# Performance work log

Hardware: AMD Instinct MI355X
Metric: run time of the kernel (lower is better)

The kernel has to match this reference:

```python
import jax, jax.numpy as jnp
import numpy as np

N = 50000          # nodes
E = 800000         # edges
D_IN, D_HID, D_OUT = 256, 128, 64
NUM_GRAPHS = 16
BN_EPS = 1e-5


def gcn_conv(x, src, dst, W, b, n_nodes):
    """PyG GCNConv: add self-loops, sym-normalized aggregation, then bias."""
    loop = jnp.arange(n_nodes, dtype=src.dtype)
    s = jnp.concatenate([src, loop])
    d = jnp.concatenate([dst, loop])
    deg = jax.ops.segment_sum(jnp.ones_like(s, dtype=x.dtype), d, num_segments=n_nodes)
    dinv = jax.lax.rsqrt(jnp.maximum(deg, 1.0))  # deg >= 1 due to self-loops
    norm = dinv[s] * dinv[d]                      # [E+N]
    h = x @ W                                     # [N, out]
    msg = h[s] * norm[:, None]                    # gather + scale
    out = jax.ops.segment_sum(msg, d, num_segments=n_nodes)
    return out + b


def batch_norm(x, gamma, beta):
    mu = jnp.mean(x, axis=0)
    var = jnp.mean(jnp.square(x - mu), axis=0)
    return (x - mu) * jax.lax.rsqrt(var + BN_EPS) * gamma + beta


def setup_inputs() -> dict:
    key = jax.random.key(0)
    ks = jax.random.split(key, 10)
    x = jax.random.normal(ks[0], (N, D_IN), dtype=jnp.float32)
    edge_index = jax.random.randint(ks[1], (2, E), 0, N, dtype=jnp.int64)
    batch = jnp.sort(jax.random.randint(ks[2], (N,), 0, NUM_GRAPHS, dtype=jnp.int64))
    def glorot(k, fan_in, fan_out):
        lim = np.sqrt(6.0 / (fan_in + fan_out))
        return jax.random.uniform(k, (fan_in, fan_out), jnp.float32, -lim, lim)
    return {
        "x": x, "edge_index": edge_index, "batch": batch,
        "W1": glorot(ks[3], D_IN, D_HID),  "b1": jnp.zeros((D_HID,), jnp.float32),
        "W2": glorot(ks[4], D_HID, D_HID), "b2": jnp.zeros((D_HID,), jnp.float32),
        "W3": glorot(ks[5], D_HID, D_OUT), "b3": jnp.zeros((D_OUT,), jnp.float32),
        "g1": jnp.ones((D_HID,), jnp.float32), "be1": jnp.zeros((D_HID,), jnp.float32),
        "g2": jnp.ones((D_HID,), jnp.float32), "be2": jnp.zeros((D_HID,), jnp.float32),
    }


def reference(x, edge_index, batch, W1, b1, W2, b2, W3, b3, g1, be1, g2, be2):
    src, dst = edge_index[0], edge_index[1]
    n = x.shape[0]
    h = gcn_conv(x, src, dst, W1, b1, n)
    h = jax.nn.relu(batch_norm(h, g1, be1))
    h = gcn_conv(h, src, dst, W2, b2, n)
    h = jax.nn.relu(batch_norm(h, g2, be2))
    h = gcn_conv(h, src, dst, W3, b3, n)          # [N, D_OUT]
    # global mean pool over graph ids
    sums = jax.ops.segment_sum(h, batch, num_segments=NUM_GRAPHS)
    cnts = jax.ops.segment_sum(jnp.ones((n,), h.dtype), batch, num_segments=NUM_GRAPHS)
    return sums / jnp.maximum(cnts, 1.0)[:, None]  # [NUM_GRAPHS, D_OUT]
```

## Files before the change

kernel.cpp:

```cpp
#include <hip/hip_runtime.h>
#include <hip/hip_bf16.h>

#define D_IN   256
#define D_HID  128
#define D_OUT_ 64
#define NGRAPH 16
#define BN_EPS 1e-5f

#define SCAN_TPB 256
#define SCAN_VPT 4

typedef __attribute__((ext_vector_type(8))) short short8;
typedef __attribute__((ext_vector_type(4))) float floatx4;

__device__ __forceinline__ unsigned short f2bf(float x) {
    unsigned u = __float_as_uint(x);
    return (unsigned short)((u + 0x7fffu + ((u >> 16) & 1u)) >> 16);
}
__device__ __forceinline__ unsigned pack2bf(float lo, float hi) {
    return (unsigned)f2bf(lo) | ((unsigned)f2bf(hi) << 16);
}
__device__ __forceinline__ void bf2_decode(unsigned u, float& lo, float& hi) {
    lo = __uint_as_float(u << 16);
    hi = __uint_as_float(u & 0xffff0000u);
}
__device__ __forceinline__ void add8(float* acc, uint4 qv) {
    float f0,f1,f2,f3,f4,f5,f6,f7;
    bf2_decode(qv.x, f0, f1); bf2_decode(qv.y, f2, f3);
    bf2_decode(qv.z, f4, f5); bf2_decode(qv.w, f6, f7);
    acc[0]+=f0; acc[1]+=f1; acc[2]+=f2; acc[3]+=f3;
    acc[4]+=f4; acc[5]+=f5; acc[6]+=f6; acc[7]+=f7;
}

__global__ void prep_count_kernel(const float* __restrict__ W1, const float* __restrict__ W2,
                                  const float* __restrict__ W3,
                                  unsigned short* __restrict__ Wt1,
                                  unsigned short* __restrict__ Wt2,
                                  unsigned short* __restrict__ Wt3, int WB,
                                  const int* __restrict__ dst, int E,
                                  int* __restrict__ deg, int* __restrict__ rank) {
    if ((int)blockIdx.x < WB) {
        int idx = blockIdx.x * 256 + threadIdx.x;
        const int S1 = D_IN * D_HID;
        const int S2 = D_HID * D_HID;
        const int S3 = D_HID * D_OUT_;
        if (idx < S1) {
            int k = idx / D_HID, n = idx - k * D_HID;
            Wt1[(size_t)n * D_IN + k] = f2bf(W1[idx]);
        } else if (idx < S1 + S2) {
            int i = idx - S1;
            int k = i / D_HID, n = i - k * D_HID;
            Wt2[(size_t)n * D_HID + k] = f2bf(W2[i]);
        } else if (idx < S1 + S2 + S3) {
            int i = idx - S1 - S2;
            int k = i / D_OUT_, n = i - k * D_OUT_;
            Wt3[(size_t)n * D_HID + k] = f2bf(W3[i]);
        }
    } else {
        int e0 = ((int)blockIdx.x - WB) * (256 * 4) + threadIdx.x;
        int d[4];
        #pragma unroll
        for (int i = 0; i < 4; ++i) {
            int e = e0 + i * 256;
            if (e < E) d[i] = dst[e];
        }
        #pragma unroll
        for (int i = 0; i < 4; ++i) {
            int e = e0 + i * 256;
            if (e < E) rank[e] = atomicAdd(&deg[d[i]], 1);
        }
    }
}

__global__ void dinv_bsum_kernel(const int* __restrict__ deg, int N,
                                 float* __restrict__ dinv, int* __restrict__ bsum) {
    __shared__ int red[SCAN_TPB];
    int t = threadIdx.x;
    int base = blockIdx.x * (SCAN_TPB * SCAN_VPT) + t;
    int s = 0;
    #pragma unroll
    for (int i = 0; i < SCAN_VPT; ++i) {
        int idx = base + i * SCAN_TPB;
        if (idx < N) {
            int d = deg[idx];
            dinv[idx] = rsqrtf((float)(d + 1));
            s += d;
        }
    }
    red[t] = s;
    __syncthreads();
    for (int off = SCAN_TPB / 2; off > 0; off >>= 1) {
        if (t < off) red[t] += red[t + off];
        __syncthreads();
    }
    if (t == 0) bsum[blockIdx.x] = red[0];
}

__global__ void scan_bsum_kernel(const int* __restrict__ bsum, int NB,
                                 int* __restrict__ bprefix,
                                 int* __restrict__ rowstart, int N, int E) {
    __shared__ int part[SCAN_TPB];
    int t = threadIdx.x;
    int s = (t < NB) ? bsum[t] : 0;
    part[t] = s;
    __syncthreads();
    for (int off = 1; off < SCAN_TPB; off <<= 1) {
        int x = (t >= off) ? part[t - off] : 0;
        __syncthreads();
        part[t] += x;
        __syncthreads();
    }
    if (t < NB) bprefix[t] = part[t] - s;
    if (t == 0) rowstart[N] = E;
}

__global__ void local_scan_kernel(const int* __restrict__ deg, int N,
                                  const int* __restrict__ bprefix,
                                  int* __restrict__ rowstart) {
    __shared__ int part[SCAN_TPB];
    int t = threadIdx.x;
    int base = blockIdx.x * (SCAN_TPB * SCAN_VPT) + t * SCAN_VPT;
    int v[SCAN_VPT];
    int s = 0;
    #pragma unroll
    for (int i = 0; i < SCAN_VPT; ++i) {
        v[i] = (base + i < N) ? deg[base + i] : 0;
        s += v[i];
    }
    part[t] = s;
    __syncthreads();
    for (int off = 1; off < SCAN_TPB; off <<= 1) {
        int x = (t >= off) ? part[t - off] : 0;
        __syncthreads();
        part[t] += x;
        __syncthreads();
    }
    int excl = part[t] - s + bprefix[blockIdx.x];
    #pragma unroll
    for (int i = 0; i < SCAN_VPT; ++i) {
        if (base + i < N) rowstart[base + i] = excl;
        excl += v[i];
    }
}

__global__ void scatter_kernel(const int* __restrict__ src, const int* __restrict__ dst,
                               int E, const int* __restrict__ rowstart,
                               const int* __restrict__ rank, int* __restrict__ csr) {
    int e0 = blockIdx.x * (256 * 4) + threadIdx.x;
    int d[4], rk[4], sv[4], pos[4];
    #pragma unroll
    for (int i = 0; i < 4; ++i) {
        int e = e0 + i * 256;
        if (e < E) { d[i] = dst[e]; rk[i] = rank[e]; sv[i] = src[e]; }
    }
    #pragma unroll
    for (int i = 0; i < 4; ++i) {
        int e = e0 + i * 256;
        if (e < E) pos[i] = rowstart[d[i]];
    }
    #pragma unroll
    for (int i = 0; i < 4; ++i) {
        int e = e0 + i * 256;
        if (e < E) csr[pos[i] + rk[i]] = sv[i];
    }
}

template<int K, int NOUT, int FUSE, int ABF16>
__device__ __forceinline__ void gemm_body(
        int bid, const void* __restrict__ Aptr, const unsigned short* __restrict__ Wt,
        unsigned short* __restrict__ Cb, int M, const float* __restrict__ dscale,
        const float* __restrict__ sums, const float* __restrict__ sumsq,
        const float* __restrict__ gam, const float* __restrict__ bet, float invN) {
    constexpr int NT = NOUT / 16;
    constexpr int KS = K / 32;
    constexpr int CHUNKS = NOUT * K / 8;
    constexpr int KROW16 = K / 8;
    __shared__ unsigned short s_wt[NOUT * K];
    __shared__ float s_sc[FUSE ? K : 1];
    __shared__ float s_sh[FUSE ? K : 1];

    int lane = threadIdx.x & 63;
    int wave = threadIdx.x >> 6;
    int col  = lane & 15;
    int quad = lane >> 4;
    int kq   = quad * 8;
    int row  = bid * 64 + wave * 16 + col;
    int rowc = min(row, M - 1);

    uint4  qa[ABF16 ? KS : 1];
    float4 a0[ABF16 ? 1 : KS], a1[ABF16 ? 1 : KS];
    if (ABF16) {
        const unsigned short* Ab = (const unsigned short*)Aptr;
        #pragma unroll
        for (int i = 0; i < KS; ++i)
            qa[i] = *(const uint4*)&Ab[(size_t)rowc * K + i * 32 + kq];
    } else {
        const float* Af = (const float*)Aptr;
        #pragma unroll
        for (int i = 0; i < KS; ++i) {
            a0[i] = *(const float4*)&Af[(size_t)rowc * K + i * 32 + kq];
            a1[i] = *(const float4*)&Af[(size_t)rowc * K + i * 32 + kq + 4];
        }
    }

    {
        const uint4* Wg = (const uint4*)Wt;
        #pragma unroll
        for (int it = 0; it < CHUNKS / 256; ++it) {
            int c = it * 256 + (int)threadIdx.x;
            uint4 v = Wg[c];
            int n = c / KROW16;
            unsigned byte = ((unsigned)c * 16u) ^ ((unsigned)(n & 7) << 4);
            *(uint4*)((char*)s_wt + byte) = v;
        }
    }
    if (FUSE) {
        int t = threadIdx.x;
        if (t < K) {
            float mu  = sums[t] * invN;
            float var = sumsq[t] * invN - mu * mu;
            float sc  = gam[t] * rsqrtf(var + BN_EPS);
            s_sc[t] = sc;
            s_sh[t] = fmaf(-mu, sc, bet[t]);
        }
    }
    __syncthreads();

    short8 afr[KS];
    if (ABF16) {
        #pragma unroll
        for (int i = 0; i < KS; ++i) {
            if (FUSE) {
                int kb = i * 32 + kq;
                float f0,f1,f2,f3,f4,f5,f6,f7;
                bf2_decode(qa[i].x, f0, f1); bf2_decode(qa[i].y, f2, f3);
                bf2_decode(qa[i].z, f4, f5); bf2_decode(qa[i].w, f6, f7);
                float4 sc0 = *(const float4*)&s_sc[kb];
                float4 sc1 = *(const float4*)&s_sc[kb + 4];
                float4 sh0 = *(const float4*)&s_sh[kb];
                float4 sh1 = *(const float4*)&s_sh[kb + 4];
                f0 = fmaxf(0.f, fmaf(f0, sc0.x, sh0.x));
                f1 = fmaxf(0.f, fmaf(f1, sc0.y, sh0.y));
                f2 = fmaxf(0.f, fmaf(f2, sc0.z, sh0.z));
                f3 = fmaxf(0.f, fmaf(f3, sc0.w, sh0.w));
                f4 = fmaxf(0.f, fmaf(f4, sc1.x, sh1.x));
                f5 = fmaxf(0.f, fmaf(f5, sc1.y, sh1.y));
                f6 = fmaxf(0.f, fmaf(f6, sc1.z, sh1.z));
                f7 = fmaxf(0.f, fmaf(f7, sc1.w, sh1.w));
                uint4 p;
                p.x = pack2bf(f0, f1); p.y = pack2bf(f2, f3);
                p.z = pack2bf(f4, f5); p.w = pack2bf(f6, f7);
                afr[i] = __builtin_bit_cast(short8, p);
            } else {
                afr[i] = __builtin_bit_cast(short8, qa[i]);
            }
        }
    } else {
        #pragma unroll
        for (int i = 0; i < KS; ++i) {
            uint4 p;
            p.x = pack2bf(a0[i].x, a0[i].y); p.y = pack2bf(a0[i].z, a0[i].w);
            p.z = pack2bf(a1[i].x, a1[i].y); p.w = pack2bf(a1[i].z, a1[i].w);
            afr[i] = __builtin_bit_cast(short8, p);
        }
    }

    floatx4 acc[NT];
    #pragma unroll
    for (int nt = 0; nt < NT; ++nt) acc[nt] = (floatx4){0.f, 0.f, 0.f, 0.f};

    #pragma unroll
    for (int i = 0; i < KS; ++i) {
        #pragma unroll
        for (int nt = 0; nt < NT; ++nt) {
            unsigned byte = ((unsigned)((nt * 16 + col) * K + i * 32 + kq)) * 2u;
            byte ^= (unsigned)(col & 7) << 4;
            short8 bfrag = *(const short8*)((const char*)s_wt + byte);
            acc[nt] = __builtin_amdgcn_mfma_f32_16x16x32_bf16(afr[i], bfrag, acc[nt], 0, 0, 0);
        }
    }

    int obase = bid * 64 + wave * 16 + quad * 4;
    #pragma unroll
    for (int r = 0; r < 4; ++r) {
        int orow = obase + r;
        if (orow < M) {
            float ds = dscale[orow];
            #pragma unroll
            for (int nt = 0; nt < NT; ++nt)
                Cb[(size_t)orow * NOUT + nt * 16 + col] = f2bf(acc[nt][r] * ds);
        }
    }
}

template<int K, int NOUT, int FUSE, int ABF16>
__global__ __launch_bounds__(256, 2) void gemm_mfma_kernel(
        const void* __restrict__ Aptr, const unsigned short* __restrict__ Wt,
        unsigned short* __restrict__ Cb, int M, const float* __restrict__ dscale,
        const float* __restrict__ sums, const float* __restrict__ sumsq,
        const float* __restrict__ gam, const float* __restrict__ bet, float invN) {
    gemm_body<K, NOUT, FUSE, ABF16>(blockIdx.x, Aptr, Wt, Cb, M, dscale,
                                    sums, sumsq, gam, bet, invN);
}

template<int D>
__global__ __launch_bounds__(256) void agg_bf16_kernel(
        const unsigned short* __restrict__ h, const float* __restrict__ dinv,
        const int* __restrict__ rowstart, const int* __restrict__ csr,
        const float* __restrict__ bias,
        unsigned short* __restrict__ outb, int N) {
    constexpr int LPR = D / 8;
    constexpr int RPB = 256 / LPR;
    int lane = threadIdx.x & (LPR - 1);
    int r    = threadIdx.x / LPR;
    int v = blockIdx.x * RPB + r;
    if (v >= N) return;
    int c0 = lane * 8;
    const unsigned short* hc = h + c0;
    float dv = dinv[v];

    float acc[8] = {0.f,0.f,0.f,0.f,0.f,0.f,0.f,0.f};
    add8(acc, *(const uint4*)&hc[(size_t)v * D]);

    int j  = rowstart[v];
    int j1 = rowstart[v + 1];
    for (; j + 8 <= j1; j += 8) {
        int   s[8]; uint4 q[8];
        #pragma unroll
        for (int i = 0; i < 8; ++i) s[i] = csr[j + i];
        #pragma unroll
        for (int i = 0; i < 8; ++i) q[i] = *(const uint4*)&hc[(size_t)s[i] * D];
        #pragma unroll
        for (int i = 0; i < 8; ++i) add8(acc, q[i]);
    }
    for (; j + 4 <= j1; j += 4) {
        int s0 = csr[j],     s1 = csr[j + 1];
        int s2 = csr[j + 2], s3 = csr[j + 3];
        uint4 q0 = *(const uint4*)&hc[(size_t)s0 * D];
        uint4 q1 = *(const uint4*)&hc[(size_t)s1 * D];
        uint4 q2 = *(const uint4*)&hc[(size_t)s2 * D];
        uint4 q3 = *(const uint4*)&hc[(size_t)s3 * D];
        add8(acc, q0); add8(acc, q1); add8(acc, q2); add8(acc, q3);
    }
    for (; j < j1; ++j) {
        int s = csr[j];
        add8(acc, *(const uint4*)&hc[(size_t)s * D]);
    }

    float4 b0 = *(const float4*)&bias[c0];
    float4 b1 = *(const float4*)&bias[c0 + 4];
    float o0 = fmaf(acc[0], dv, b0.x), o1 = fmaf(acc[1], dv, b0.y);
    float o2 = fmaf(acc[2], dv, b0.z), o3 = fmaf(acc[3], dv, b0.w);
    float o4 = fmaf(acc[4], dv, b1.x), o5 = fmaf(acc[5], dv, b1.y);
    float o6 = fmaf(acc[6], dv, b1.z), o7 = fmaf(acc[7], dv, b1.w);
    uint4 o;
    o.x = pack2bf(o0, o1); o.y = pack2bf(o2, o3);
    o.z = pack2bf(o4, o5); o.w = pack2bf(o6, o7);
    *(uint4*)&outb[(size_t)v * D + c0] = o;
}

__global__ void bn_stats_bf16_kernel(const unsigned short* __restrict__ x, int N,
                                     float* __restrict__ sums, float* __restrict__ sumsq) {
    __shared__ float ls0[256], ls1[256], lq0[256], lq1[256];
    int pr = threadIdx.x & 63;
    int rg = threadIdx.x >> 6;
    float s0=0.f, s1=0.f, q0=0.f, q1=0.f;
    for (int v = blockIdx.x * 4 + rg; v < N; v += gridDim.x * 4) {
        unsigned u = *(const unsigned*)&x[(size_t)v * 128 + pr * 2];
        float lo, hi; bf2_decode(u, lo, hi);
        s0 += lo; s1 += hi;
        q0 = fmaf(lo, lo, q0); q1 = fmaf(hi, hi, q1);
    }
    ls0[threadIdx.x]=s0; ls1[threadIdx.x]=s1; lq0[threadIdx.x]=q0; lq1[threadIdx.x]=q1;
    __syncthreads();
    if (threadIdx.x < 64) {
        int pp = threadIdx.x;
        float a0=0,a1=0,b0=0,b1=0;
        #pragma unroll
        for (int g = 0; g < 4; ++g) {
            a0 += ls0[g*64+pp]; a1 += ls1[g*64+pp];
            b0 += lq0[g*64+pp]; b1 += lq1[g*64+pp];
        }
        atomicAdd(&sums[pp*2],  a0); atomicAdd(&sums[pp*2+1],  a1);
        atomicAdd(&sumsq[pp*2], b0); atomicAdd(&sumsq[pp*2+1], b1);
    }
}

__global__ void pool_bf16_kernel(const unsigned short* __restrict__ x,
                                 const int* __restrict__ batch, int N,
                                 float* __restrict__ psum, int* __restrict__ pcnt) {
    __shared__ float ls[NGRAPH * 64];
    __shared__ int   lc[NGRAPH];
    for (int i = threadIdx.x; i < NGRAPH * 64; i += blockDim.x) ls[i] = 0.f;
    if (threadIdx.x < NGRAPH) lc[threadIdx.x] = 0;
    __syncthreads();
    int total = N * 32;
    for (int idx = blockIdx.x * blockDim.x + threadIdx.x; idx < total;
         idx += gridDim.x * blockDim.x) {
        int v = idx >> 5, cp = idx & 31;
        unsigned u = *(const unsigned*)&x[(size_t)v * 64 + cp * 2];
        float lo, hi; bf2_decode(u, lo, hi);
        int g = batch[v];
        atomicAdd(&ls[g * 64 + cp * 2],     lo);
        atomicAdd(&ls[g * 64 + cp * 2 + 1], hi);
        if (cp == 0) atomicAdd(&lc[g], 1);
    }
    __syncthreads();
    for (int i = threadIdx.x; i < NGRAPH * 64; i += blockDim.x) atomicAdd(&psum[i], ls[i]);
    if (threadIdx.x < NGRAPH) atomicAdd(&pcnt[threadIdx.x], lc[threadIdx.x]);
}

__global__ void pool_final_kernel(const float* __restrict__ psum, const int* __restrict__ pcnt,
                                  float* __restrict__ out) {
    int i = threadIdx.x;
    int g = i >> 6;
    float cnt = (float)max(pcnt[g], 1);
    out[i] = psum[i] / cnt;
}

extern "C" void kernel_launch(void* const* d_in, const int* in_sizes, int n_in,
                              void* d_out, int out_size, void* d_ws, size_t ws_size,
                              hipStream_t stream) {
    const float* x   = (const float*)d_in[0];
    const int*   ei  = (const int*)d_in[1];
    const int*   bat = (const int*)d_in[2];
    const float* W1  = (const float*)d_in[3];
    const float* b1  = (const float*)d_in[4];
    const float* W2  = (const float*)d_in[5];
    const float* b2  = (const float*)d_in[6];
    const float* W3  = (const float*)d_in[7];
    const float* b3  = (const float*)d_in[8];
    const float* g1  = (const float*)d_in[9];
    const float* be1 = (const float*)d_in[10];
    const float* g2  = (const float*)d_in[11];
    const float* be2 = (const float*)d_in[12];
    float* out = (float*)d_out;

    int N = in_sizes[0] / D_IN;
    int E = in_sizes[1] / 2;
    const int* src = ei;
    const int* dst = ei + E;

    char* p = (char*)d_ws;
    auto alloc = [&](size_t bytes) { char* r = p; p += (bytes + 255) & ~(size_t)255; return r; };
    int NB = (N + SCAN_TPB * SCAN_VPT - 1) / (SCAN_TPB * SCAN_VPT);
    char*  zbase    = p;
    int*   deg      = (int*)  alloc((size_t)N * 4);
    float* sums1    = (float*)alloc(128 * 4);
    float* sumsq1   = (float*)alloc(128 * 4);
    float* sums2    = (float*)alloc(128 * 4);
    float* sumsq2   = (float*)alloc(128 * 4);
    float* psum     = (float*)alloc(NGRAPH * 64 * 4);
    int*   pcnt     = (int*)  alloc(NGRAPH * 4);
    size_t zspan    = (size_t)(p - zbase);
    int*   rowstart = (int*)  alloc((size_t)(N + 1) * 4);
    int*   rank     = (int*)  alloc((size_t)E * 4);
    float* dinv     = (float*)alloc((size_t)N * 4);
    int*   bsum     = (int*)  alloc((size_t)NB * 4);
    int*   bprefix  = (int*)  alloc((size_t)NB * 4);
    int*   csr      = (int*)  alloc((size_t)E * 4);
    unsigned short* hb16   = (unsigned short*)alloc((size_t)N * 128 * 2);
    unsigned short* aggb16 = (unsigned short*)alloc((size_t)N * 128 * 2);
    unsigned short* Wt1 = (unsigned short*)alloc((size_t)D_HID * D_IN * 2);
    unsigned short* Wt2 = (unsigned short*)alloc((size_t)D_HID * D_HID * 2);
    unsigned short* Wt3 = (unsigned short*)alloc((size_t)D_OUT_ * D_HID * 2);

    int ebl4 = (E + 1023) / 1024;
    int gblocks = (N + 63) / 64;
    float invN = 1.0f / (float)N;
    int wtot = D_IN * D_HID + D_HID * D_HID + D_HID * D_OUT_;
    int WB = (wtot + 255) / 256;

    (void)hipMemsetAsync(zbase, 0, zspan, stream);
    prep_count_kernel<<<WB + ebl4, 256, 0, stream>>>(W1, W2, W3, Wt1, Wt2, Wt3,
                                                     WB, dst, E, deg, rank);

    dinv_bsum_kernel<<<NB, SCAN_TPB, 0, stream>>>(deg, N, dinv, bsum);
    scan_bsum_kernel<<<1, SCAN_TPB, 0, stream>>>(bsum, NB, bprefix, rowstart, N, E);
    local_scan_kernel<<<NB, SCAN_TPB, 0, stream>>>(deg, N, bprefix, rowstart);
    scatter_kernel<<<ebl4, 256, 0, stream>>>(src, dst, E, rowstart, rank, csr);

    gemm_mfma_kernel<D_IN, D_HID, 0, 0><<<gblocks, 256, 0, stream>>>(
        x, Wt1, hb16, N, dinv, nullptr, nullptr, nullptr, nullptr, 0.f);
    agg_bf16_kernel<D_HID><<<(N + 15) / 16, 256, 0, stream>>>(
        hb16, dinv, rowstart, csr, b1, aggb16, N);
    bn_stats_bf16_kernel<<<256, 256, 0, stream>>>(aggb16, N, sums1, sumsq1);

    gemm_mfma_kernel<D_HID, D_HID, 1, 1><<<gblocks, 256, 0, stream>>>(
        aggb16, Wt2, hb16, N, dinv, sums1, sumsq1, g1, be1, invN);
    agg_bf16_kernel<D_HID><<<(N + 15) / 16, 256, 0, stream>>>(
        hb16, dinv, rowstart, csr, b2, aggb16, N);
    bn_stats_bf16_kernel<<<256, 256, 0, stream>>>(aggb16, N, sums2, sumsq2);

    gemm_mfma_kernel<D_HID, D_OUT_, 1, 1><<<gblocks, 256, 0, stream>>>(
        aggb16, Wt3, hb16, N, dinv, sums2, sumsq2, g2, be2, invN);
    agg_bf16_kernel<D_OUT_><<<(N + 31) / 32, 256, 0, stream>>>(
        hb16, dinv, rowstart, csr, b3, aggb16, N);

    pool_bf16_kernel<<<256, 256, 0, stream>>>(aggb16, bat, N, psum, pcnt);
    pool_final_kernel<<<1, NGRAPH * 64, 0, stream>>>(psum, pcnt, out);
}
```

Before: 348.9 us.

## Merge three-pass degree scan into one kernel and fold pool finalize into pool

```diff
diff --git a/kernel.cpp b/kernel.cpp
--- a/kernel.cpp
+++ b/kernel.cpp
@@ -72,75 +72,59 @@
     }
 }
 
-__global__ void dinv_bsum_kernel(const int* __restrict__ deg, int N,
-                                 float* __restrict__ dinv, int* __restrict__ bsum) {
+__global__ void scan_all_kernel(const int* __restrict__ deg, int N, int E,
+                                float* __restrict__ dinv, int* __restrict__ rowstart) {
     __shared__ int red[SCAN_TPB];
     int t = threadIdx.x;
-    int base = blockIdx.x * (SCAN_TPB * SCAN_VPT) + t;
-    int s = 0;
-    #pragma unroll
-    for (int i = 0; i < SCAN_VPT; ++i) {
-        int idx = base + i * SCAN_TPB;
-        if (idx < N) {
-            int d = deg[idx];
-            dinv[idx] = rsqrtf((float)(d + 1));
-            s += d;
-        }
-    }
-    red[t] = s;
+    int blockStart = blockIdx.x * (SCAN_TPB * SCAN_VPT);
+
+    int ps = 0;
+    const int4* d4 = (const int4*)deg;
+    for (int i = t; i < (blockStart >> 2); i += SCAN_TPB) {
+        int4 q = d4[i];
+        ps += q.x + q.y + q.z + q.w;
+    }
+    red[t] = ps;
     __syncthreads();
     for (int off = SCAN_TPB / 2; off > 0; off >>= 1) {
         if (t < off) red[t] += red[t + off];
         __syncthreads();
     }
-    if (t == 0) bsum[blockIdx.x] = red[0];
-}
-
-__global__ void scan_bsum_kernel(const int* __restrict__ bsum, int NB,
-                                 int* __restrict__ bprefix,
-                                 int* __restrict__ rowstart, int N, int E) {
-    __shared__ int part[SCAN_TPB];
-    int t = threadIdx.x;
-    int s = (t < NB) ? bsum[t] : 0;
-    part[t] = s;
-    __syncthreads();
-    for (int off = 1; off < SCAN_TPB; off <<= 1) {
-        int x = (t >= off) ? part[t - off] : 0;
-        __syncthreads();
-        part[t] += x;
-        __syncthreads();
-    }
-    if (t < NB) bprefix[t] = part[t] - s;
-    if (t == 0) rowstart[N] = E;
-}
-
-__global__ void local_scan_kernel(const int* __restrict__ deg, int N,
-                                  const int* __restrict__ bprefix,
-                                  int* __restrict__ rowstart) {
-    __shared__ int part[SCAN_TPB];
-    int t = threadIdx.x;
-    int base = blockIdx.x * (SCAN_TPB * SCAN_VPT) + t * SCAN_VPT;
+    int bprefix = red[0];
+    __syncthreads();
+
+    int base = blockStart + t * SCAN_VPT;
     int v[SCAN_VPT];
     int s = 0;
+    if (base < N) {
+        int4 q = d4[base >> 2];
+        v[0] = q.x; v[1] = q.y; v[2] = q.z; v[3] = q.w;
+        #pragma unroll
+        for (int i = 0; i < SCAN_VPT; ++i) {
+            if (base + i >= N) v[i] = 0;
+            s += v[i];
+        }
+    } else {
+        v[0]=v[1]=v[2]=v[3]=0;
+    }
+    red[t] = s;
+    __syncthreads();
+    for (int off = 1; off < SCAN_TPB; off <<= 1) {
+        int x = (t >= off) ? red[t - off] : 0;
+        __syncthreads();
+        red[t] += x;
+        __syncthreads();
+    }
+    int excl = red[t] - s + bprefix;
     #pragma unroll
     for (int i = 0; i < SCAN_VPT; ++i) {
-        v[i] = (base + i < N) ? deg[base + i] : 0;
-        s += v[i];
-    }
-    part[t] = s;
-    __syncthreads();
-    for (int off = 1; off < SCAN_TPB; off <<= 1) {
-        int x = (t >= off) ? part[t - off] : 0;
-        __syncthreads();
-        part[t] += x;
-        __syncthreads();
-    }
-    int excl = part[t] - s + bprefix[blockIdx.x];
-    #pragma unroll
-    for (int i = 0; i < SCAN_VPT; ++i) {
-        if (base + i < N) rowstart[base + i] = excl;
+        if (base + i < N) {
+            rowstart[base + i] = excl;
+            dinv[base + i] = rsqrtf((float)(v[i] + 1));
+        }
         excl += v[i];
     }
+    if (blockIdx.x == 0 && t == 0) rowstart[N] = E;
 }
 
 __global__ void scatter_kernel(const int* __restrict__ src, const int* __restrict__ dst,
@@ -388,9 +372,11 @@
 
 __global__ void pool_bf16_kernel(const unsigned short* __restrict__ x,
                                  const int* __restrict__ batch, int N,
-                                 float* __restrict__ psum, int* __restrict__ pcnt) {
+                                 float* __restrict__ psum, int* __restrict__ pcnt,
+                                 int* __restrict__ done, float* __restrict__ out) {
     __shared__ float ls[NGRAPH * 64];
     __shared__ int   lc[NGRAPH];
+    __shared__ int   s_last;
     for (int i = threadIdx.x; i < NGRAPH * 64; i += blockDim.x) ls[i] = 0.f;
     if (threadIdx.x < NGRAPH) lc[threadIdx.x] = 0;
     __syncthreads();
@@ -408,14 +394,18 @@
     __syncthreads();
     for (int i = threadIdx.x; i < NGRAPH * 64; i += blockDim.x) atomicAdd(&psum[i], ls[i]);
     if (threadIdx.x < NGRAPH) atomicAdd(&pcnt[threadIdx.x], lc[threadIdx.x]);
-}
-
-__global__ void pool_final_kernel(const float* __restrict__ psum, const int* __restrict__ pcnt,
-                                  float* __restrict__ out) {
-    int i = threadIdx.x;
-    int g = i >> 6;
-    float cnt = (float)max(pcnt[g], 1);
-    out[i] = psum[i] / cnt;
+
+    __threadfence();
+    if (threadIdx.x == 0) s_last = (atomicAdd(done, 1) == (int)gridDim.x - 1);
+    __syncthreads();
+    if (s_last) {
+        for (int i = threadIdx.x; i < NGRAPH * 64; i += blockDim.x) {
+            int g = i >> 6;
+            float sv = atomicAdd(&psum[i], 0.f);
+            int   cv = atomicAdd(&pcnt[g], 0);
+            out[i] = sv / (float)max(cv, 1);
+        }
+    }
 }
 
 extern "C" void kernel_launch(void* const* d_in, const int* in_sizes, int n_in,
@@ -452,12 +442,11 @@
     float* sumsq2   = (float*)alloc(128 * 4);
     float* psum     = (float*)alloc(NGRAPH * 64 * 4);
     int*   pcnt     = (int*)  alloc(NGRAPH * 4);
+    int*   pdone    = (int*)  alloc(4);
     size_t zspan    = (size_t)(p - zbase);
     int*   rowstart = (int*)  alloc((size_t)(N + 1) * 4);
     int*   rank     = (int*)  alloc((size_t)E * 4);
     float* dinv     = (float*)alloc((size_t)N * 4);
-    int*   bsum     = (int*)  alloc((size_t)NB * 4);
-    int*   bprefix  = (int*)  alloc((size_t)NB * 4);
     int*   csr      = (int*)  alloc((size_t)E * 4);
     unsigned short* hb16   = (unsigned short*)alloc((size_t)N * 128 * 2);
     unsigned short* aggb16 = (unsigned short*)alloc((size_t)N * 128 * 2);
@@ -475,9 +464,7 @@
     prep_count_kernel<<<WB + ebl4, 256, 0, stream>>>(W1, W2, W3, Wt1, Wt2, Wt3,
                                                      WB, dst, E, deg, rank);
 
-    dinv_bsum_kernel<<<NB, SCAN_TPB, 0, stream>>>(deg, N, dinv, bsum);
-    scan_bsum_kernel<<<1, SCAN_TPB, 0, stream>>>(bsum, NB, bprefix, rowstart, N, E);
-    local_scan_kernel<<<NB, SCAN_TPB, 0, stream>>>(deg, N, bprefix, rowstart);
+    scan_all_kernel<<<NB, SCAN_TPB, 0, stream>>>(deg, N, E, dinv, rowstart);
     scatter_kernel<<<ebl4, 256, 0, stream>>>(src, dst, E, rowstart, rank, csr);
 
     gemm_mfma_kernel<D_IN, D_HID, 0, 0><<<gblocks, 256, 0, stream>>>(
@@ -497,6 +484,5 @@
     agg_bf16_kernel<D_OUT_><<<(N + 31) / 32, 256, 0, stream>>>(
         hb16, dinv, rowstart, csr, b3, aggb16, N);
 
-    pool_bf16_kernel<<<256, 256, 0, stream>>>(aggb16, bat, N, psum, pcnt);
-    pool_final_kernel<<<1, NGRAPH * 64, 0, stream>>>(psum, pcnt, out);
-}
+    pool_bf16_kernel<<<256, 256, 0, stream>>>(aggb16, bat, N, psum, pcnt, pdone, out);
+}
```

New measurement: 360.8 us. +3.4%, slower.

## Fuse BatchNorm statistics into aggregation kernel with replicated atomic accumulators

Applied to the files above, without the earlier changes.

```diff
diff --git a/kernel.cpp b/kernel.cpp
--- a/kernel.cpp
+++ b/kernel.cpp
@@ -6,6 +6,7 @@
 #define D_OUT_ 64
 #define NGRAPH 16
 #define BN_EPS 1e-5f
+#define BNC    64
 
 #define SCAN_TPB 256
 #define SCAN_VPT 4
@@ -217,8 +218,14 @@
     if (FUSE) {
         int t = threadIdx.x;
         if (t < K) {
-            float mu  = sums[t] * invN;
-            float var = sumsq[t] * invN - mu * mu;
+            float s = 0.f, q = 0.f;
+            #pragma unroll 8
+            for (int c = 0; c < BNC; ++c) {
+                s += sums[c * K + t];
+                q += sumsq[c * K + t];
+            }
+            float mu  = s * invN;
+            float var = q * invN - mu * mu;
             float sc  = gam[t] * rsqrtf(var + BN_EPS);
             s_sc[t] = sc;
             s_sh[t] = fmaf(-mu, sc, bet[t]);
@@ -303,27 +310,31 @@
                                     sums, sumsq, gam, bet, invN);
 }
 
-template<int D>
+template<int D, int BNS>
 __global__ __launch_bounds__(256) void agg_bf16_kernel(
         const unsigned short* __restrict__ h, const float* __restrict__ dinv,
         const int* __restrict__ rowstart, const int* __restrict__ csr,
         const float* __restrict__ bias,
-        unsigned short* __restrict__ outb, int N) {
+        unsigned short* __restrict__ outb, int N,
+        float* __restrict__ sums, float* __restrict__ sumsq) {
+    static_assert(!BNS || D == 128, "BNS path assumes LPR=16 (4 rows/wave)");
     constexpr int LPR = D / 8;
     constexpr int RPB = 256 / LPR;
     int lane = threadIdx.x & (LPR - 1);
     int r    = threadIdx.x / LPR;
     int v = blockIdx.x * RPB + r;
-    if (v >= N) return;
+    bool valid = v < N;
+    if (!BNS && !valid) return;
+    int vc = valid ? v : N - 1;
     int c0 = lane * 8;
     const unsigned short* hc = h + c0;
-    float dv = dinv[v];
+    float dv = dinv[vc];
 
     float acc[8] = {0.f,0.f,0.f,0.f,0.f,0.f,0.f,0.f};
-    add8(acc, *(const uint4*)&hc[(size_t)v * D]);
-
-    int j  = rowstart[v];
-    int j1 = rowstart[v + 1];
+    add8(acc, *(const uint4*)&hc[(size_t)vc * D]);
+
+    int j  = rowstart[vc];
+    int j1 = valid ? rowstart[vc + 1] : j;
     for (; j + 8 <= j1; j += 8) {
         int   s[8]; uint4 q[8];
         #pragma unroll
@@ -349,40 +360,41 @@
 
     float4 b0 = *(const float4*)&bias[c0];
     float4 b1 = *(const float4*)&bias[c0 + 4];
-    float o0 = fmaf(acc[0], dv, b0.x), o1 = fmaf(acc[1], dv, b0.y);
-    float o2 = fmaf(acc[2], dv, b0.z), o3 = fmaf(acc[3], dv, b0.w);
-    float o4 = fmaf(acc[4], dv, b1.x), o5 = fmaf(acc[5], dv, b1.y);
-    float o6 = fmaf(acc[6], dv, b1.z), o7 = fmaf(acc[7], dv, b1.w);
-    uint4 o;
-    o.x = pack2bf(o0, o1); o.y = pack2bf(o2, o3);
-    o.z = pack2bf(o4, o5); o.w = pack2bf(o6, o7);
-    *(uint4*)&outb[(size_t)v * D + c0] = o;
-}
-
-__global__ void bn_stats_bf16_kernel(const unsigned short* __restrict__ x, int N,
-                                     float* __restrict__ sums, float* __restrict__ sumsq) {
-    __shared__ float ls0[256], ls1[256], lq0[256], lq1[256];
-    int pr = threadIdx.x & 63;
-    int rg = threadIdx.x >> 6;
-    float s0=0.f, s1=0.f, q0=0.f, q1=0.f;
-    for (int v = blockIdx.x * 4 + rg; v < N; v += gridDim.x * 4) {
-        unsigned u = *(const unsigned*)&x[(size_t)v * 128 + pr * 2];
-        float lo, hi; bf2_decode(u, lo, hi);
-        s0 += lo; s1 += hi;
-        q0 = fmaf(lo, lo, q0); q1 = fmaf(hi, hi, q1);
-    }
-    ls0[threadIdx.x]=s0; ls1[threadIdx.x]=s1; lq0[threadIdx.x]=q0; lq1[threadIdx.x]=q1;
-    __syncthreads();
-    if (threadIdx.x < 64) {
-        int pp = threadIdx.x;
-        float a0=0,a1=0,b0=0,b1=0;
-        #pragma unroll
-        for (int g = 0; g < 4; ++g) {
-            a0 += ls0[g*64+pp]; a1 += ls1[g*64+pp];
-            b0 += lq0[g*64+pp]; b1 += lq1[g*64+pp];
-        }
-        atomicAdd(&sums[pp*2],  a0); atomicAdd(&sums[pp*2+1],  a1);
-        atomicAdd(&sumsq[pp*2], b0); atomicAdd(&sumsq[pp*2+1], b1);
+    float o[8];
+    o[0] = fmaf(acc[0], dv, b0.x); o[1] = fmaf(acc[1], dv, b0.y);
+    o[2] = fmaf(acc[2], dv, b0.z); o[3] = fmaf(acc[3], dv, b0.w);
+    o[4] = fmaf(acc[4], dv, b1.x); o[5] = fmaf(acc[5], dv, b1.y);
+    o[6] = fmaf(acc[6], dv, b1.z); o[7] = fmaf(acc[7], dv, b1.w);
+    if (valid) {
+        uint4 ov;
+        ov.x = pack2bf(o[0], o[1]); ov.y = pack2bf(o[2], o[3]);
+        ov.z = pack2bf(o[4], o[5]); ov.w = pack2bf(o[6], o[7]);
+        *(uint4*)&outb[(size_t)v * D + c0] = ov;
+    }
+
+    if (BNS) {
+        float sv[8], qv[8];
+        #pragma unroll
+        for (int i = 0; i < 8; ++i) {
+            sv[i] = valid ? o[i] : 0.f;
+            qv[i] = valid ? o[i] * o[i] : 0.f;
+        }
+        #pragma unroll
+        for (int i = 0; i < 8; ++i) {
+            sv[i] += __shfl_xor(sv[i], 16); sv[i] += __shfl_xor(sv[i], 32);
+            qv[i] += __shfl_xor(qv[i], 16); qv[i] += __shfl_xor(qv[i], 32);
+        }
+        if ((threadIdx.x & 48) == 0) {
+            int l = threadIdx.x & 15;
+            int copy = (int)blockIdx.x & (BNC - 1);
+            float* sp = sums  + copy * 128 + l * 8;
+            float* qp = sumsq + copy * 128 + l * 8;
+            #pragma unroll
+            for (int i = 0; i < 8; ++i) {
+                atomicAdd(&sp[i], sv[i]);
+                atomicAdd(&qp[i], qv[i]);
+            }
+        }
     }
 }
 
@@ -446,10 +458,10 @@
     int NB = (N + SCAN_TPB * SCAN_VPT - 1) / (SCAN_TPB * SCAN_VPT);
     char*  zbase    = p;
     int*   deg      = (int*)  alloc((size_t)N * 4);
-    float* sums1    = (float*)alloc(128 * 4);
-    float* sumsq1   = (float*)alloc(128 * 4);
-    float* sums2    = (float*)alloc(128 * 4);
-    float* sumsq2   = (float*)alloc(128 * 4);
+    float* sums1    = (float*)alloc((size_t)BNC * 128 * 4);
+    float* sumsq1   = (float*)alloc((size_t)BNC * 128 * 4);
+    float* sums2    = (float*)alloc((size_t)BNC * 128 * 4);
+    float* sumsq2   = (float*)alloc((size_t)BNC * 128 * 4);
     float* psum     = (float*)alloc(NGRAPH * 64 * 4);
     int*   pcnt     = (int*)  alloc(NGRAPH * 4);
     size_t zspan    = (size_t)(p - zbase);
@@ -482,20 +494,18 @@
 
     gemm_mfma_kernel<D_IN, D_HID, 0, 0><<<gblocks, 256, 0, stream>>>(
         x, Wt1, hb16, N, dinv, nullptr, nullptr, nullptr, nullptr, 0.f);
-    agg_bf16_kernel<D_HID><<<(N + 15) / 16, 256, 0, stream>>>(
-        hb16, dinv, rowstart, csr, b1, aggb16, N);
-    bn_stats_bf16_kernel<<<256, 256, 0, stream>>>(aggb16, N, sums1, sumsq1);
+    agg_bf16_kernel<D_HID, 1><<<(N + 15) / 16, 256, 0, stream>>>(
+        hb16, dinv, rowstart, csr, b1, aggb16, N, sums1, sumsq1);
 
     gemm_mfma_kernel<D_HID, D_HID, 1, 1><<<gblocks, 256, 0, stream>>>(
         aggb16, Wt2, hb16, N, dinv, sums1, sumsq1, g1, be1, invN);
-    agg_bf16_kernel<D_HID><<<(N + 15) / 16, 256, 0, stream>>>(
-        hb16, dinv, rowstart, csr, b2, aggb16, N);
-    bn_stats_bf16_kernel<<<256, 256, 0, stream>>>(aggb16, N, sums2, sumsq2);
+    agg_bf16_kernel<D_HID, 1><<<(N + 15) / 16, 256, 0, stream>>>(
+        hb16, dinv, rowstart, csr, b2, aggb16, N, sums2, sumsq2);
 
     gemm_mfma_kernel<D_HID, D_OUT_, 1, 1><<<gblocks, 256, 0, stream>>>(
         aggb16, Wt3, hb16, N, dinv, sums2, sumsq2, g2, be2, invN);
-    agg_bf16_kernel<D_OUT_><<<(N + 31) / 32, 256, 0, stream>>>(
-        hb16, dinv, rowstart, csr, b3, aggb16, N);
+    agg_bf16_kernel<D_OUT_, 0><<<(N + 31) / 32, 256, 0, stream>>>(
+        hb16, dinv, rowstart, csr, b3, aggb16, N, nullptr, nullptr);
 
     pool_bf16_kernel<<<256, 256, 0, stream>>>(aggb16, bat, N, psum, pcnt);
     pool_final_kernel<<<1, NGRAPH * 64, 0, stream>>>(psum, pcnt, out);
```

Result: slower. 500.9 us (+43.6%).
